# Kernel tuning notes

Measured on AMD Instinct MI355X. Metric: run time of the kernel, lower is better.

Reference implementation:

```python
import jax, jax.numpy as jnp
import numpy as np

E = 16        # n_routed_experts
D = 2048      # in_features
H = 1024      # d_intermediate per routed expert
K = 4         # n_activated_experts
SH = 1024     # shared expert hidden = n_shared_experts * d_intermediate
T = 2048      # tokens


def gated_mlp(x, w1, w2):
    # fc1 -> chunk -> y * silu(gate) -> fc2   (bias-free, as in mamba GatedMLP)
    y = x @ w1.T                      # [T, 2h]
    y, gate = jnp.split(y, 2, axis=-1)
    return (y * jax.nn.silu(gate)) @ w2.T


def setup_inputs() -> dict:
    key = jax.random.key(0)
    ks = jax.random.split(key, 6)
    s = 0.02  # init scale so softmax scores are well-behaved
    return {
        "x": jax.random.normal(ks[0], (T, D), jnp.float32),
        "gate_w": jax.random.normal(ks[1], (E, D), jnp.float32) * s,
        "w1": jax.random.normal(ks[2], (E, 2 * H, D), jnp.float32) * s,
        "w2": jax.random.normal(ks[3], (E, D, H), jnp.float32) * s,
        "sw1": jax.random.normal(ks[4], (2 * SH, D), jnp.float32) * s,
        "sw2": jax.random.normal(ks[5], (D, SH), jnp.float32) * s,
    }


def reference(x, gate_w, w1, w2, sw1, sw2):
    # ---- Gate (softmax scores in fp32, no bias, single expert group) ----
    scores = jax.nn.softmax((x @ gate_w.T).astype(jnp.float32), axis=-1)  # [T, E]
    top_vals, top_idx = jax.lax.top_k(scores, K)                          # [T, K]
    weights = top_vals.astype(x.dtype)  # route_scale = 1.0

    # Per-token routing weight per expert, [T, E]. topk indices are distinct
    # per token, matching `z[idx] += expert(x[idx]) * weights[idx, top]`.
    t_idx = jnp.arange(x.shape[0])[:, None]
    tok_w = jnp.zeros((x.shape[0], E), x.dtype).at[t_idx, top_idx].add(weights)

    # ---- Routed experts: accumulate weighted expert outputs ----
    def body(z, ew):
        w1_e, w2_e, we = ew  # [2H,D], [D,H], [T]
        return z + gated_mlp(x, w1_e, w2_e) * we[:, None], None

    z, _ = jax.lax.scan(body, jnp.zeros_like(x), (w1, w2, tok_w.T))

    # ---- Shared expert added to all tokens ----
    return z + gated_mlp(x, sw1, sw2)
```

## Files before the change

### kernel.cpp

```cpp
#include <hip/hip_runtime.h>
#include <stdint.h>

#define T_TOK 2048
#define D_IN  2048
#define H_I   1024
#define NE    16
#define TOPK  4
#define TWOH  2048
#define MAX_SLOTS 12288

typedef __attribute__((ext_vector_type(8))) __bf16 bf16x8;
typedef __attribute__((ext_vector_type(4))) float  f32x4;

__device__ __forceinline__ unsigned short f2bf(float f) {
  unsigned u = __float_as_uint(f);
  u += 0x7FFF + ((u >> 16) & 1);
  return (unsigned short)(u >> 16);
}
__device__ __forceinline__ float bf2f(unsigned short s) {
  return __uint_as_float(((unsigned)s) << 16);
}

__device__ __forceinline__ void group_meta(const int* __restrict__ cnt, int g,
                                           int& base, int& pc, int& shared_base) {
  int o = 0; base = 0; pc = T_TOK;
  for (int e = 0; e < NE; ++e) {
    int pce = (cnt[e] + 127) & ~127;
    if (e == g) { base = o; pc = pce; }
    o += pce;
  }
  shared_base = o;
  if (g == 16) base = o;
}

#define GLDS16(gp, lp) __builtin_amdgcn_global_load_lds( \
    (__attribute__((address_space(1))) void*)(gp),       \
    (__attribute__((address_space(3))) void*)(lp), 16, 0, 0)

#define R_X   1048576
#define R_W1  (R_X + 16777216)
#define R_W2  (R_W1 + 8388608)
#define R_SW1 (R_W2 + 1048576)
#define R_SW2 (R_SW1 + 524288)
__global__ void cvt_all(const float4* __restrict__ x,  const float4* __restrict__ w1,
                        const float4* __restrict__ w2, const float4* __restrict__ sw1,
                        const float4* __restrict__ sw2,
                        ushort4* __restrict__ xd,  ushort4* __restrict__ w1d,
                        ushort4* __restrict__ w2d, ushort4* __restrict__ sw1d,
                        ushort4* __restrict__ sw2d, int* __restrict__ cnt) {
  int i = blockIdx.x * 256 + threadIdx.x;
  if (i < NE) cnt[i] = 0;
  const float4* s; ushort4* d; int j;
  if      (i < R_X)   { s = x;   d = xd;   j = i; }
  else if (i < R_W1)  { s = w1;  d = w1d;  j = i - R_X; }
  else if (i < R_W2)  { s = w2;  d = w2d;  j = i - R_W1; }
  else if (i < R_SW1) { s = sw1; d = sw1d; j = i - R_W2; }
  else if (i < R_SW2) { s = sw2; d = sw2d; j = i - R_SW1; }
  else return;
  float4 f = s[j];
  ushort4 u;
  u.x = f2bf(f.x); u.y = f2bf(f.y); u.z = f2bf(f.z); u.w = f2bf(f.w);
  d[j] = u;
}

__global__ __launch_bounds__(256) void gate_topk(
    const float* __restrict__ x, const float* __restrict__ gw,
    int* __restrict__ cnt, int* __restrict__ cap_tok, float* __restrict__ cap_w,
    int* __restrict__ tk_ep)
{
  int t = blockIdx.x;
  const float* xr = x + (size_t)t * D_IN;
  float acc[NE];
#pragma unroll
  for (int e = 0; e < NE; ++e) acc[e] = 0.f;
  for (int d = threadIdx.x; d < D_IN; d += 256) {
    float xv = xr[d];
#pragma unroll
    for (int e = 0; e < NE; ++e) acc[e] += xv * gw[e * D_IN + d];
  }
#pragma unroll
  for (int e = 0; e < NE; ++e) {
    float v = acc[e];
#pragma unroll
    for (int o = 32; o > 0; o >>= 1) v += __shfl_down(v, o, 64);
    acc[e] = v;
  }
  __shared__ float red[4][NE];
  int wv = threadIdx.x >> 6, ln = threadIdx.x & 63;
  if (ln == 0) {
#pragma unroll
    for (int e = 0; e < NE; ++e) red[wv][e] = acc[e];
  }
  __syncthreads();
  if (threadIdx.x == 0) {
    float lg[NE];
    float mx = -1e30f;
#pragma unroll
    for (int e = 0; e < NE; ++e) {
      lg[e] = red[0][e] + red[1][e] + red[2][e] + red[3][e];
      mx = fmaxf(mx, lg[e]);
    }
    float s = 0.f;
#pragma unroll
    for (int e = 0; e < NE; ++e) { lg[e] = __expf(lg[e] - mx); s += lg[e]; }
    float inv = 1.f / s;
    bool used[NE] = {};
    for (int k = 0; k < TOPK; ++k) {
      float best = -1.f; int bi = 0;
      for (int e = 0; e < NE; ++e)
        if (!used[e] && lg[e] > best) { best = lg[e]; bi = e; }
      used[bi] = true;
      int pos = atomicAdd(&cnt[bi], 1);
      cap_tok[bi * T_TOK + pos] = t;
      cap_w[bi * T_TOK + pos]   = best * inv;
      tk_ep[t * TOPK + k] = (bi << 16) | pos;
    }
  }
}

__global__ void compact_lists(const int* __restrict__ cnt,
                              const int* __restrict__ cap_tok, const float* __restrict__ cap_w,
                              const int* __restrict__ tk_ep,
                              int* __restrict__ stok, float* __restrict__ swt,
                              int* __restrict__ tok2slot)
{
  int idx = blockIdx.x * 256 + threadIdx.x;
  if (idx < NE * T_TOK) {
    int e = idx >> 11, pos = idx & (T_TOK - 1);
    int base, pc, sb;
    group_meta(cnt, e, base, pc, sb);
    if (pos < pc) {
      int dst = base + pos;
      if (pos < cnt[e]) { stok[dst] = cap_tok[idx]; swt[dst] = cap_w[idx]; }
      else              { stok[dst] = 0;            swt[dst] = 0.f; }
    }
  } else if (idx < NE * T_TOK + T_TOK) {
    int t = idx - NE * T_TOK;
    int base, pc, sb;
    group_meta(cnt, 16, base, pc, sb);
    stok[base + t] = t; swt[base + t] = 1.f;
  } else {
    int j = idx - NE * T_TOK - T_TOK;
    int ep = tk_ep[j];
    int e = ep >> 16;
    int base, pc, sb;
    group_meta(cnt, e, base, pc, sb);
    tok2slot[j] = base + (ep & 0xFFFF);
  }
}

__global__ __launch_bounds__(256) void fc1_fused(
    const unsigned short* __restrict__ xbf,
    const unsigned short* __restrict__ w1bf,
    const unsigned short* __restrict__ sw1bf,
    const int* __restrict__ stok, const float* __restrict__ swt,
    const int* __restrict__ cnt,
    unsigned short* __restrict__ hbuf)
{
  int bx = blockIdx.x;
  int g = bx >> 8;
  int rem = bx & 255;
  int mt = rem >> 4, nt = rem & 15;
  int base, pc, sb;
  group_meta(cnt, g, base, pc, sb);
  if (mt * 128 >= pc) return;
  int base_slot = base + mt * 128;
  const unsigned short* B = (g == 16) ? sw1bf : w1bf + (size_t)g * TWOH * D_IN;

  __shared__ __align__(16) unsigned char smem[32768];
  auto sA = (unsigned short (*)[128][8])smem;
  auto sB = (unsigned short (*)[128][8])(smem + 16384);
  auto sG = (float (*)[64])smem;

  int tid = threadIdx.x;
  int w = tid >> 6, l = tid & 63;
  int lm = l & 15, q = l >> 4;
  int wm = w >> 1, wn = w & 1;

  const unsigned short* a0 = xbf + (size_t)stok[base_slot + l]      * D_IN + w * 16;
  const unsigned short* a1 = xbf + (size_t)stok[base_slot + 64 + l] * D_IN + w * 16;
  const unsigned short* b0 = B + (size_t)(nt * 64 + l)       * D_IN + w * 16;
  const unsigned short* b1 = B + (size_t)(H_I + nt * 64 + l) * D_IN + w * 16;

  f32x4 acc[4][4];
#pragma unroll
  for (int i = 0; i < 4; ++i)
#pragma unroll
    for (int j = 0; j < 4; ++j) acc[i][j] = (f32x4){0.f, 0.f, 0.f, 0.f};

  for (int kt = 0; kt < D_IN; kt += 64) {
    GLDS16(a0 + kt,     &sA[2 * w][0][0]);
    GLDS16(a0 + kt + 8, &sA[2 * w + 1][0][0]);
    GLDS16(a1 + kt,     &sA[2 * w][64][0]);
    GLDS16(a1 + kt + 8, &sA[2 * w + 1][64][0]);
    GLDS16(b0 + kt,     &sB[2 * w][0][0]);
    GLDS16(b0 + kt + 8, &sB[2 * w + 1][0][0]);
    GLDS16(b1 + kt,     &sB[2 * w][64][0]);
    GLDS16(b1 + kt + 8, &sB[2 * w + 1][64][0]);
    __syncthreads();
    bf16x8 af[2][4], bfr[2][4];
#pragma unroll
    for (int s = 0; s < 2; ++s) {
#pragma unroll
      for (int i = 0; i < 4; ++i) af[s][i]  = *(const bf16x8*)&sA[4 * s + q][wm * 64 + i * 16 + lm][0];
#pragma unroll
      for (int j = 0; j < 4; ++j) bfr[s][j] = *(const bf16x8*)&sB[4 * s + q][wn * 64 + j * 16 + lm][0];
    }
#pragma unroll
    for (int s = 0; s < 2; ++s)
#pragma unroll
      for (int i = 0; i < 4; ++i)
#pragma unroll
        for (int j = 0; j < 4; ++j)
          acc[i][j] = __builtin_amdgcn_mfma_f32_16x16x32_bf16(af[s][i], bfr[s][j], acc[i][j], 0, 0, 0);
    __syncthreads();
  }

  if (wn == 1) {
#pragma unroll
    for (int i = 0; i < 4; ++i)
#pragma unroll
      for (int r = 0; r < 4; ++r) {
        int row = wm * 64 + i * 16 + q * 4 + r;
        int sw = (row & 3) << 4;
#pragma unroll
        for (int j = 0; j < 4; ++j) {
          float gv = acc[i][j][r];
          sG[row][(j * 16 + lm) ^ sw] = gv / (1.f + __expf(-gv));
        }
      }
  }
  __syncthreads();
  if (wn == 0) {
#pragma unroll
    for (int i = 0; i < 4; ++i)
#pragma unroll
      for (int r = 0; r < 4; ++r) {
        int row = wm * 64 + i * 16 + q * 4 + r;
        int slot = base_slot + row;
        float wt = swt[slot];
        int sw = (row & 3) << 4;
        unsigned short* hrow = hbuf + (size_t)slot * H_I + nt * 64;
#pragma unroll
        for (int j = 0; j < 4; ++j) {
          int col = j * 16 + lm;
          hrow[col] = f2bf(acc[i][j][r] * sG[row][col ^ sw] * wt);
        }
      }
  }
}

__global__ __launch_bounds__(256) void fc2_gemm(
    const unsigned short* __restrict__ hbuf,
    const unsigned short* __restrict__ w2bf,
    const unsigned short* __restrict__ sw2bf,
    const int* __restrict__ cnt,
    unsigned short* __restrict__ Yout)
{
  int bx = blockIdx.x;
  int g = bx >> 8;
  int rem = bx & 255;
  int mt = rem >> 4, nt = rem & 15;
  int base, pc, sb;
  group_meta(cnt, g, base, pc, sb);
  if (mt * 128 >= pc) return;
  int base_slot = base + mt * 128;
  const unsigned short* B = (g == 16) ? sw2bf : w2bf + (size_t)g * D_IN * H_I;

  __shared__ __align__(16) unsigned short sA[8][128][8];
  __shared__ __align__(16) unsigned short sB[8][128][8];

  int tid = threadIdx.x;
  int w = tid >> 6, l = tid & 63;
  int lm = l & 15, q = l >> 4;
  int wm = w >> 1, wn = w & 1;

  const unsigned short* a0 = hbuf + (size_t)(base_slot + l)      * H_I + w * 16;
  const unsigned short* a1 = hbuf + (size_t)(base_slot + 64 + l) * H_I + w * 16;
  const unsigned short* b0 = B + (size_t)(nt * 128 + l)      * H_I + w * 16;
  const unsigned short* b1 = B + (size_t)(nt * 128 + 64 + l) * H_I + w * 16;

  f32x4 acc[4][4];
#pragma unroll
  for (int i = 0; i < 4; ++i)
#pragma unroll
    for (int j = 0; j < 4; ++j) acc[i][j] = (f32x4){0.f, 0.f, 0.f, 0.f};

  for (int kt = 0; kt < H_I; kt += 64) {
    GLDS16(a0 + kt,     &sA[2 * w][0][0]);
    GLDS16(a0 + kt + 8, &sA[2 * w + 1][0][0]);
    GLDS16(a1 + kt,     &sA[2 * w][64][0]);
    GLDS16(a1 + kt + 8, &sA[2 * w + 1][64][0]);
    GLDS16(b0 + kt,     &sB[2 * w][0][0]);
    GLDS16(b0 + kt + 8, &sB[2 * w + 1][0][0]);
    GLDS16(b1 + kt,     &sB[2 * w][64][0]);
    GLDS16(b1 + kt + 8, &sB[2 * w + 1][64][0]);
    __syncthreads();
    bf16x8 af[2][4], bfr[2][4];
#pragma unroll
    for (int s = 0; s < 2; ++s) {
#pragma unroll
      for (int i = 0; i < 4; ++i) af[s][i]  = *(const bf16x8*)&sA[4 * s + q][wm * 64 + i * 16 + lm][0];
#pragma unroll
      for (int j = 0; j < 4; ++j) bfr[s][j] = *(const bf16x8*)&sB[4 * s + q][wn * 64 + j * 16 + lm][0];
    }
#pragma unroll
    for (int s = 0; s < 2; ++s)
#pragma unroll
      for (int i = 0; i < 4; ++i)
#pragma unroll
        for (int j = 0; j < 4; ++j)
          acc[i][j] = __builtin_amdgcn_mfma_f32_16x16x32_bf16(af[s][i], bfr[s][j], acc[i][j], 0, 0, 0);
    __syncthreads();
  }

  int colbase = nt * 128 + wn * 64;
#pragma unroll
  for (int i = 0; i < 4; ++i) {
#pragma unroll
    for (int r = 0; r < 4; ++r) {
      int row = wm * 64 + i * 16 + q * 4 + r;
      unsigned short* orow = Yout + (size_t)(base_slot + row) * D_IN + colbase + lm;
#pragma unroll
      for (int j = 0; j < 4; ++j)
        orow[j * 16] = f2bf(acc[i][j][r]);
    }
  }
}

__global__ __launch_bounds__(256) void reduce_out(
    const unsigned short* __restrict__ Yout, const int* __restrict__ tok2slot,
    const int* __restrict__ cnt, float4* __restrict__ out)
{
  int idx = blockIdx.x * 256 + threadIdx.x;
  int t = idx >> 9, c = (idx & 511) << 2;
  int sb = 0;
  for (int e = 0; e < NE; ++e) sb += (cnt[e] + 127) & ~127;
  int sl[5];
  sl[0] = sb + t;
#pragma unroll
  for (int k = 0; k < TOPK; ++k) sl[k + 1] = tok2slot[t * TOPK + k];
  float4 a = {0.f, 0.f, 0.f, 0.f};
#pragma unroll
  for (int k = 0; k < 5; ++k) {
    ushort4 v = *(const ushort4*)(Yout + (size_t)sl[k] * D_IN + c);
    a.x += bf2f(v.x); a.y += bf2f(v.y); a.z += bf2f(v.z); a.w += bf2f(v.w);
  }
  out[idx] = a;
}

extern "C" void kernel_launch(void* const* d_in, const int* in_sizes, int n_in,
                              void* d_out, int out_size, void* d_ws, size_t ws_size,
                              hipStream_t stream)
{
  const float* x   = (const float*)d_in[0];
  const float* gw  = (const float*)d_in[1];
  const float* w1  = (const float*)d_in[2];
  const float* w2  = (const float*)d_in[3];
  const float* sw1 = (const float*)d_in[4];
  const float* sw2 = (const float*)d_in[5];
  float* out = (float*)d_out;

  char* ws = (char*)d_ws;
  size_t off = 0;
  auto alloc = [&](size_t bytes) -> char* {
    char* p = ws + off; off += (bytes + 255) & ~(size_t)255; return p;
  };
  unsigned short* xbf   = (unsigned short*)alloc((size_t)T_TOK * D_IN * 2);
  unsigned short* w1bf  = (unsigned short*)alloc((size_t)NE * TWOH * D_IN * 2);
  unsigned short* w2bf  = (unsigned short*)alloc((size_t)NE * D_IN * H_I * 2);
  unsigned short* sw1bf = (unsigned short*)alloc((size_t)TWOH * D_IN * 2);
  unsigned short* sw2bf = (unsigned short*)alloc((size_t)D_IN * H_I * 2);
  unsigned short* hbuf  = (unsigned short*)alloc((size_t)MAX_SLOTS * H_I * 2);
  int*   cnt    = (int*)alloc(NE * 4);
  int*   captok = (int*)alloc((size_t)NE * T_TOK * 4);
  float* capw   = (float*)alloc((size_t)NE * T_TOK * 4);
  int*   stok   = (int*)alloc(MAX_SLOTS * 4);
  float* swt    = (float*)alloc(MAX_SLOTS * 4);
  int*   tk_ep  = (int*)alloc((size_t)T_TOK * TOPK * 4);
  int*   t2s    = (int*)alloc((size_t)T_TOK * TOPK * 4);
  if (off > ws_size) return;

  unsigned short* Yout = (unsigned short*)w1bf;

  cvt_all<<<(R_SW2 + 255) / 256, 256, 0, stream>>>(
      (const float4*)x, (const float4*)w1, (const float4*)w2,
      (const float4*)sw1, (const float4*)sw2,
      (ushort4*)xbf, (ushort4*)w1bf, (ushort4*)w2bf, (ushort4*)sw1bf, (ushort4*)sw2bf, cnt);

  gate_topk<<<T_TOK, 256, 0, stream>>>(x, gw, cnt, captok, capw, tk_ep);
  compact_lists<<<(NE * T_TOK + T_TOK + TOPK * T_TOK) / 256, 256, 0, stream>>>(
      cnt, captok, capw, tk_ep, stok, swt, t2s);
  fc1_fused<<<17 * 256, 256, 0, stream>>>(xbf, w1bf, sw1bf, stok, swt, cnt, hbuf);
  fc2_gemm<<<17 * 256, 256, 0, stream>>>(hbuf, w2bf, sw2bf, cnt, Yout);
  reduce_out<<<(T_TOK * 512) / 256, 256, 0, stream>>>(Yout, t2s, cnt, (float4*)out);
}
```

Baseline: 899.3 us.

## Double-buffer LDS tiles in fc1 and fc2 GEMM main loops

Both grouped GEMM kernels now use two 32KB LDS buffers, issuing the global-to-LDS loads for the next K tile before computing MFMAs on the current one. Only one barrier is kept per iteration. The aim is to overlap global memory latency with matrix compute. In exchange LDS use per block doubles to 64KB, which may lower occupancy.

```diff
diff --git a/kernel.cpp b/kernel.cpp
--- a/kernel.cpp
+++ b/kernel.cpp
@@ -167,9 +167,7 @@
   int base_slot = base + mt * 128;
   const unsigned short* B = (g == 16) ? sw1bf : w1bf + (size_t)g * TWOH * D_IN;
 
-  __shared__ __align__(16) unsigned char smem[32768];
-  auto sA = (unsigned short (*)[128][8])smem;
-  auto sB = (unsigned short (*)[128][8])(smem + 16384);
+  __shared__ __align__(16) unsigned char smem[65536];
   auto sG = (float (*)[64])smem;
 
   int tid = threadIdx.x;
@@ -188,31 +186,45 @@
 #pragma unroll
     for (int j = 0; j < 4; ++j) acc[i][j] = (f32x4){0.f, 0.f, 0.f, 0.f};
 
+#define STAGE_FC1(BUF, KT) do {                                                  \
+    auto sA_ = (unsigned short (*)[128][8])(smem + ((BUF) << 15));               \
+    auto sB_ = (unsigned short (*)[128][8])(smem + ((BUF) << 15) + 16384);       \
+    GLDS16(a0 + (KT),     &sA_[2 * w][0][0]);                                    \
+    GLDS16(a0 + (KT) + 8, &sA_[2 * w + 1][0][0]);                                \
+    GLDS16(a1 + (KT),     &sA_[2 * w][64][0]);                                   \
+    GLDS16(a1 + (KT) + 8, &sA_[2 * w + 1][64][0]);                               \
+    GLDS16(b0 + (KT),     &sB_[2 * w][0][0]);                                    \
+    GLDS16(b0 + (KT) + 8, &sB_[2 * w + 1][0][0]);                                \
+    GLDS16(b1 + (KT),     &sB_[2 * w][64][0]);                                   \
+    GLDS16(b1 + (KT) + 8, &sB_[2 * w + 1][64][0]);                               \
+  } while (0)
+
+#define COMPUTE_FC1(BUF) do {                                                    \
+    auto sA_ = (unsigned short (*)[128][8])(smem + ((BUF) << 15));               \
+    auto sB_ = (unsigned short (*)[128][8])(smem + ((BUF) << 15) + 16384);       \
+    bf16x8 af[2][4], bfr[2][4];                                                  \
+    _Pragma("unroll")                                                            \
+    for (int s = 0; s < 2; ++s) {                                                \
+      _Pragma("unroll")                                                          \
+      for (int i = 0; i < 4; ++i) af[s][i]  = *(const bf16x8*)&sA_[4 * s + q][wm * 64 + i * 16 + lm][0]; \
+      _Pragma("unroll")                                                          \
+      for (int j = 0; j < 4; ++j) bfr[s][j] = *(const bf16x8*)&sB_[4 * s + q][wn * 64 + j * 16 + lm][0]; \
+    }                                                                            \
+    _Pragma("unroll")                                                            \
+    for (int s = 0; s < 2; ++s)                                                  \
+      _Pragma("unroll")                                                          \
+      for (int i = 0; i < 4; ++i)                                                \
+        _Pragma("unroll")                                                        \
+        for (int j = 0; j < 4; ++j)                                              \
+          acc[i][j] = __builtin_amdgcn_mfma_f32_16x16x32_bf16(af[s][i], bfr[s][j], acc[i][j], 0, 0, 0); \
+  } while (0)
+
+  STAGE_FC1(0, 0);
+  __syncthreads();
   for (int kt = 0; kt < D_IN; kt += 64) {
-    GLDS16(a0 + kt,     &sA[2 * w][0][0]);
-    GLDS16(a0 + kt + 8, &sA[2 * w + 1][0][0]);
-    GLDS16(a1 + kt,     &sA[2 * w][64][0]);
-    GLDS16(a1 + kt + 8, &sA[2 * w + 1][64][0]);
-    GLDS16(b0 + kt,     &sB[2 * w][0][0]);
-    GLDS16(b0 + kt + 8, &sB[2 * w + 1][0][0]);
-    GLDS16(b1 + kt,     &sB[2 * w][64][0]);
-    GLDS16(b1 + kt + 8, &sB[2 * w + 1][64][0]);
-    __syncthreads();
-    bf16x8 af[2][4], bfr[2][4];
-#pragma unroll
-    for (int s = 0; s < 2; ++s) {
-#pragma unroll
-      for (int i = 0; i < 4; ++i) af[s][i]  = *(const bf16x8*)&sA[4 * s + q][wm * 64 + i * 16 + lm][0];
-#pragma unroll
-      for (int j = 0; j < 4; ++j) bfr[s][j] = *(const bf16x8*)&sB[4 * s + q][wn * 64 + j * 16 + lm][0];
-    }
-#pragma unroll
-    for (int s = 0; s < 2; ++s)
-#pragma unroll
-      for (int i = 0; i < 4; ++i)
-#pragma unroll
-        for (int j = 0; j < 4; ++j)
-          acc[i][j] = __builtin_amdgcn_mfma_f32_16x16x32_bf16(af[s][i], bfr[s][j], acc[i][j], 0, 0, 0);
+    int cur = (kt >> 6) & 1;
+    if (kt + 64 < D_IN) STAGE_FC1(cur ^ 1, kt + 64);
+    COMPUTE_FC1(cur);
     __syncthreads();
   }
 
@@ -248,6 +260,8 @@
         }
       }
   }
+#undef STAGE_FC1
+#undef COMPUTE_FC1
 }
 
 __global__ __launch_bounds__(256) void fc2_gemm(
@@ -267,8 +281,7 @@
   int base_slot = base + mt * 128;
   const unsigned short* B = (g == 16) ? sw2bf : w2bf + (size_t)g * D_IN * H_I;
 
-  __shared__ __align__(16) unsigned short sA[8][128][8];
-  __shared__ __align__(16) unsigned short sB[8][128][8];
+  __shared__ __align__(16) unsigned char smem[65536];
 
   int tid = threadIdx.x;
   int w = tid >> 6, l = tid & 63;
@@ -286,31 +299,45 @@
 #pragma unroll
     for (int j = 0; j < 4; ++j) acc[i][j] = (f32x4){0.f, 0.f, 0.f, 0.f};
 
+#define STAGE_FC2(BUF, KT) do {                                                  \
+    auto sA_ = (unsigned short (*)[128][8])(smem + ((BUF) << 15));               \
+    auto sB_ = (unsigned short (*)[128][8])(smem + ((BUF) << 15) + 16384);       \
+    GLDS16(a0 + (KT),     &sA_[2 * w][0][0]);                                    \
+    GLDS16(a0 + (KT) + 8, &sA_[2 * w + 1][0][0]);                                \
+    GLDS16(a1 + (KT),     &sA_[2 * w][64][0]);                                   \
+    GLDS16(a1 + (KT) + 8, &sA_[2 * w + 1][64][0]);                               \
+    GLDS16(b0 + (KT),     &sB_[2 * w][0][0]);                                    \
+    GLDS16(b0 + (KT) + 8, &sB_[2 * w + 1][0][0]);                                \
+    GLDS16(b1 + (KT),     &sB_[2 * w][64][0]);                                   \
+    GLDS16(b1 + (KT) + 8, &sB_[2 * w + 1][64][0]);                               \
+  } while (0)
+
+#define COMPUTE_FC2(BUF) do {                                                    \
+    auto sA_ = (unsigned short (*)[128][8])(smem + ((BUF) << 15));               \
+    auto sB_ = (unsigned short (*)[128][8])(smem + ((BUF) << 15) + 16384);       \
+    bf16x8 af[2][4], bfr[2][4];                                                  \
+    _Pragma("unroll")                                                            \
+    for (int s = 0; s < 2; ++s) {                                                \
+      _Pragma("unroll")                                                          \
+      for (int i = 0; i < 4; ++i) af[s][i]  = *(const bf16x8*)&sA_[4 * s + q][wm * 64 + i * 16 + lm][0]; \
+      _Pragma("unroll")                                                          \
+      for (int j = 0; j < 4; ++j) bfr[s][j] = *(const bf16x8*)&sB_[4 * s + q][wn * 64 + j * 16 + lm][0]; \
+    }                                                                            \
+    _Pragma("unroll")                                                            \
+    for (int s = 0; s < 2; ++s)                                                  \
+      _Pragma("unroll")                                                          \
+      for (int i = 0; i < 4; ++i)                                                \
+        _Pragma("unroll")                                                        \
+        for (int j = 0; j < 4; ++j)                                              \
+          acc[i][j] = __builtin_amdgcn_mfma_f32_16x16x32_bf16(af[s][i], bfr[s][j], acc[i][j], 0, 0, 0); \
+  } while (0)
+
+  STAGE_FC2(0, 0);
+  __syncthreads();
   for (int kt = 0; kt < H_I; kt += 64) {
-    GLDS16(a0 + kt,     &sA[2 * w][0][0]);
-    GLDS16(a0 + kt + 8, &sA[2 * w + 1][0][0]);
-    GLDS16(a1 + kt,     &sA[2 * w][64][0]);
-    GLDS16(a1 + kt + 8, &sA[2 * w + 1][64][0]);
-    GLDS16(b0 + kt,     &sB[2 * w][0][0]);
-    GLDS16(b0 + kt + 8, &sB[2 * w + 1][0][0]);
-    GLDS16(b1 + kt,     &sB[2 * w][64][0]);
-    GLDS16(b1 + kt + 8, &sB[2 * w + 1][64][0]);
-    __syncthreads();
-    bf16x8 af[2][4], bfr[2][4];
-#pragma unroll
-    for (int s = 0; s < 2; ++s) {
-#pragma unroll
-      for (int i = 0; i < 4; ++i) af[s][i]  = *(const bf16x8*)&sA[4 * s + q][wm * 64 + i * 16 + lm][0];
-#pragma unroll
-      for (int j = 0; j < 4; ++j) bfr[s][j] = *(const bf16x8*)&sB[4 * s + q][wn * 64 + j * 16 + lm][0];
-    }
-#pragma unroll
-    for (int s = 0; s < 2; ++s)
-#pragma unroll
-      for (int i = 0; i < 4; ++i)
-#pragma unroll
-        for (int j = 0; j < 4; ++j)
-          acc[i][j] = __builtin_amdgcn_mfma_f32_16x16x32_bf16(af[s][i], bfr[s][j], acc[i][j], 0, 0, 0);
+    int cur = (kt >> 6) & 1;
+    if (kt + 64 < H_I) STAGE_FC2(cur ^ 1, kt + 64);
+    COMPUTE_FC2(cur);
     __syncthreads();
   }
 
@@ -326,6 +353,8 @@
         orow[j * 16] = f2bf(acc[i][j][r]);
     }
   }
+#undef STAGE_FC2
+#undef COMPUTE_FC2
 }
 
 __global__ __launch_bounds__(256) void reduce_out(
```

Measured after the change: 903.0 us. About the same (+0.4%).
